# Kernel tuning notes

Hardware: AMD Instinct MI355X
Metric: run time of the kernel (lower is better)

## Reference

```python
import jax, jax.numpy as jnp
import numpy as np

B, I, D = 512, 128, 64


def setup_inputs() -> dict:
    key = jax.random.key(0)
    embeddings = jax.random.normal(key, (B, I, D), dtype=jnp.float32)
    return {"embeddings": embeddings}


def reference(embeddings):
    # Original: em_ij[b,i,j,d] = emb[b,i,d]*emb[b,j,d]; ctx = mean over j.
    # Algebraically: ctx[b,i,d] = emb[b,i,d] * mean_j emb[b,j,d] -- linear time,
    # no [B,I,I,D] materialization.
    mean_emb = jnp.mean(embeddings, axis=1, keepdims=True)  # [B,1,D]
    ctx_vec = embeddings * mean_emb                         # [B,I,D]
    # activation_function (undefined in the snippet; repo uses a smooth
    # pointwise activation -- tanh assumed). Dropout is identity in eval mode.
    return jnp.tanh(ctx_vec)
```

## Files before the change

kernel.cpp:

```cpp
#include <hip/hip_runtime.h>


#define BB 512
#define II 128
#define DD 64
#define ELEMS_PER_BATCH (II * DD)
#define VEC_PER_BATCH   (ELEMS_PER_BATCH / 4)
#define BLOCK 256
#define VEC_PER_THREAD  (VEC_PER_BATCH / BLOCK)

__device__ __forceinline__ float fast_tanh(float x) {
    float e = __expf(2.0f * x);
    return __fmaf_rn(-2.0f, __builtin_amdgcn_rcpf(e + 1.0f), 1.0f);
}

__global__ __launch_bounds__(BLOCK) void ctx_tanh_kernel(
        const float* __restrict__ emb, float* __restrict__ out) {
    __shared__ float4 s_emb[VEC_PER_BATCH];
    __shared__ float4 s_part[BLOCK];
    __shared__ float4 s_mean[16];

    const int b = blockIdx.x;
    const int t = threadIdx.x;
    const float4* __restrict__ gin  = (const float4*)(emb + (size_t)b * ELEMS_PER_BATCH);
    float4* __restrict__       gout = (float4*)(out + (size_t)b * ELEMS_PER_BATCH);

    float4 acc = make_float4(0.f, 0.f, 0.f, 0.f);
    #pragma unroll
    for (int k = 0; k < VEC_PER_THREAD; ++k) {
        int j = t + BLOCK * k;
        float4 v = gin[j];
        s_emb[j] = v;
        acc.x += v.x; acc.y += v.y; acc.z += v.z; acc.w += v.w;
    }
    s_part[t] = acc;
    __syncthreads();

    if (t < 16) {
        float4 s = make_float4(0.f, 0.f, 0.f, 0.f);
        #pragma unroll
        for (int m = 0; m < 16; ++m) {
            float4 p = s_part[m * 16 + t];
            s.x += p.x; s.y += p.y; s.z += p.z; s.w += p.w;
        }
        const float inv = 1.0f / (float)II;
        s.x *= inv; s.y *= inv; s.z *= inv; s.w *= inv;
        s_mean[t] = s;
    }
    __syncthreads();

    #pragma unroll
    for (int k = 0; k < VEC_PER_THREAD; ++k) {
        int j = t + BLOCK * k;
        float4 v = s_emb[j];
        float4 m = s_mean[j & 15];
        float4 o;
        o.x = fast_tanh(v.x * m.x);
        o.y = fast_tanh(v.y * m.y);
        o.z = fast_tanh(v.z * m.z);
        o.w = fast_tanh(v.w * m.w);
        gout[j] = o;
    }
}

extern "C" void kernel_launch(void* const* d_in, const int* in_sizes, int n_in,
                              void* d_out, int out_size, void* d_ws, size_t ws_size,
                              hipStream_t stream) {
    const float* emb = (const float*)d_in[0];
    float* out = (float*)d_out;
    ctx_tanh_kernel<<<dim3(BB), dim3(BLOCK), 0, stream>>>(emb, out);
}
```

Measured before the change: 67.62 us.

## Keep batch tile in registers with 1024-thread blocks and nontemporal IO

Grows each block to 1024 threads so every thread holds its two float4 values in registers, removing the shared-memory staging copy of the whole batch. The column-sum reduction becomes a two-level tree in shared memory. Global loads and stores use nontemporal builtins to avoid polluting caches. The larger block may reduce scheduling flexibility and adds an extra barrier stage.

```diff
diff --git a/kernel.cpp b/kernel.cpp
--- a/kernel.cpp
+++ b/kernel.cpp
@@ -6,8 +6,9 @@
 #define DD 64
 #define ELEMS_PER_BATCH (II * DD)
 #define VEC_PER_BATCH   (ELEMS_PER_BATCH / 4)
-#define BLOCK 256
-#define VEC_PER_THREAD  (VEC_PER_BATCH / BLOCK)
+#define BLOCK 1024
+
+typedef float vf4 __attribute__((ext_vector_type(4)));
 
 __device__ __forceinline__ float fast_tanh(float x) {
     float e = __expf(2.0f * x);
@@ -16,51 +17,42 @@
 
 __global__ __launch_bounds__(BLOCK) void ctx_tanh_kernel(
         const float* __restrict__ emb, float* __restrict__ out) {
-    __shared__ float4 s_emb[VEC_PER_BATCH];
-    __shared__ float4 s_part[BLOCK];
-    __shared__ float4 s_mean[16];
+    __shared__ vf4 s_part[BLOCK];
+    __shared__ vf4 s_mean[16];
 
     const int b = blockIdx.x;
     const int t = threadIdx.x;
-    const float4* __restrict__ gin  = (const float4*)(emb + (size_t)b * ELEMS_PER_BATCH);
-    float4* __restrict__       gout = (float4*)(out + (size_t)b * ELEMS_PER_BATCH);
+    const vf4* __restrict__ gin  = (const vf4*)(emb + (size_t)b * ELEMS_PER_BATCH);
+    vf4* __restrict__       gout = (vf4*)(out + (size_t)b * ELEMS_PER_BATCH);
 
-    float4 acc = make_float4(0.f, 0.f, 0.f, 0.f);
-    #pragma unroll
-    for (int k = 0; k < VEC_PER_THREAD; ++k) {
-        int j = t + BLOCK * k;
-        float4 v = gin[j];
-        s_emb[j] = v;
-        acc.x += v.x; acc.y += v.y; acc.z += v.z; acc.w += v.w;
+    vf4 v0 = __builtin_nontemporal_load(&gin[t]);
+    vf4 v1 = __builtin_nontemporal_load(&gin[t + BLOCK]);
+
+    s_part[t] = v0 + v1;
+    __syncthreads();
+
+    if (t < 256) {
+        s_part[t] = s_part[t] + s_part[t + 256] + s_part[t + 512] + s_part[t + 768];
     }
-    s_part[t] = acc;
     __syncthreads();
 
     if (t < 16) {
-        float4 s = make_float4(0.f, 0.f, 0.f, 0.f);
+        vf4 s = (vf4)(0.0f);
         #pragma unroll
-        for (int m = 0; m < 16; ++m) {
-            float4 p = s_part[m * 16 + t];
-            s.x += p.x; s.y += p.y; s.z += p.z; s.w += p.w;
-        }
-        const float inv = 1.0f / (float)II;
-        s.x *= inv; s.y *= inv; s.z *= inv; s.w *= inv;
-        s_mean[t] = s;
+        for (int m = 0; m < 16; ++m) s += s_part[t + 16 * m];
+        s_mean[t] = s * (1.0f / (float)II);
     }
     __syncthreads();
 
-    #pragma unroll
-    for (int k = 0; k < VEC_PER_THREAD; ++k) {
-        int j = t + BLOCK * k;
-        float4 v = s_emb[j];
-        float4 m = s_mean[j & 15];
-        float4 o;
-        o.x = fast_tanh(v.x * m.x);
-        o.y = fast_tanh(v.y * m.y);
-        o.z = fast_tanh(v.z * m.z);
-        o.w = fast_tanh(v.w * m.w);
-        gout[j] = o;
-    }
+    const vf4 m = s_mean[t & 15];
+    vf4 p0 = v0 * m, p1 = v1 * m;
+    vf4 o0, o1;
+    o0.x = fast_tanh(p0.x); o0.y = fast_tanh(p0.y);
+    o0.z = fast_tanh(p0.z); o0.w = fast_tanh(p0.w);
+    o1.x = fast_tanh(p1.x); o1.y = fast_tanh(p1.y);
+    o1.z = fast_tanh(p1.z); o1.w = fast_tanh(p1.w);
+    __builtin_nontemporal_store(o0, &gout[t]);
+    __builtin_nontemporal_store(o1, &gout[t + BLOCK]);
 }
 
 extern "C" void kernel_launch(void* const* d_in, const int* in_sizes, int n_in,
```

Result: slower. 69.74 us (+3.1%).
